# Kernel tuning notes

Hardware: AMD Instinct MI355X
Metric: run time of the kernel (lower is better)

The kernel has to match this reference:

```python
import jax, jax.numpy as jnp
import numpy as np

B, N, C, H = 4, 2048, 1024, 16
HD = C // H  # head_dim = 64


def setup_inputs() -> dict:
    key = jax.random.key(0)
    ks = jax.random.split(key, 16)
    s = 0.02
    return {
        "x": jax.random.normal(ks[0], (B, N, C), dtype=jnp.float32),
        # qkv_proj: Linear(C, 3C): weight (3C, C), bias (3C,)
        "W_qkv": jax.random.normal(ks[1], (3 * C, C), dtype=jnp.float32) * s,
        "b_qkv": jax.random.normal(ks[2], (3 * C,), dtype=jnp.float32) * s,
        # out_proj: Linear(C, C)
        "W_out": jax.random.normal(ks[3], (C, C), dtype=jnp.float32) * s,
        "b_out": jax.random.normal(ks[4], (C,), dtype=jnp.float32) * s,
        # dynamically-reassigned position bias: shape (1, N, H, H) per the code's
        # (B, num_heads=N, seq_len=H, seq_len=H) score tensor
        "pos_bias": jax.random.normal(ks[5], (1, N, H, H), dtype=jnp.float32) * 0.01,
        # conv_proj: Linear(C, C)
        "W_cp": jax.random.normal(ks[6], (C, C), dtype=jnp.float32) * s,
        "b_cp": jax.random.normal(ks[7], (C,), dtype=jnp.float32) * s,
        # pointwise Conv1d(C, C, k=1): weight (C, C) after squeezing kernel dim
        "W_pw": jax.random.normal(ks[8], (C, C), dtype=jnp.float32) * s,
        "b_pw": jax.random.normal(ks[9], (C,), dtype=jnp.float32) * s,
        # depthwise Conv1d(C, C, k=3, groups=C): weight (C, 3)
        "W_dw": jax.random.normal(ks[10], (C, 3), dtype=jnp.float32) * s,
        "b_dw": jax.random.normal(ks[11], (C,), dtype=jnp.float32) * s,
        # token_wise_proj: Linear(C, C)
        "W_tw": jax.random.normal(ks[12], (C, C), dtype=jnp.float32) * s,
        "b_tw": jax.random.normal(ks[13], (C,), dtype=jnp.float32) * s,
    }


def reference(x, W_qkv, b_qkv, W_out, b_out, pos_bias, W_cp, b_cp,
              W_pw, b_pw, W_dw, b_dw, W_tw, b_tw) -> jnp.ndarray:
    Bx, Nx, Cx = x.shape
    scale = HD ** -0.5
    # qkv -> (B, N, H, 3*HD), chunk into q,k,v of (B, N, H, HD).
    # NOTE: faithful to the torch code, heads stay on axis 2; the matmul
    # contracts head_dim giving (B, N, H, H) scores (attention over heads).
    qkv = (x @ W_qkv.T + b_qkv).reshape(Bx, Nx, H, 3 * HD)
    q, k, v = jnp.split(qkv, 3, axis=-1)
    scores = jnp.einsum('bnhd,bngd->bnhg', q, k) * scale + pos_bias
    attn = jax.nn.softmax(scores, axis=-1)
    attn_out = jnp.einsum('bnhg,bngd->bnhd', attn, v).reshape(Bx, Nx, Cx)
    attn_out = attn_out @ W_out.T + b_out

    # Convolutional branch
    xc = x @ W_cp.T + b_cp          # conv_proj
    xc = xc @ W_pw.T + b_pw          # pointwise conv (k=1) == linear over channels
    xp = jnp.pad(xc, ((0, 0), (1, 1), (0, 0)))  # pad seq for k=3, padding=1
    xc = (xp[:, :-2] * W_dw[:, 0] + xp[:, 1:-1] * W_dw[:, 1]
          + xp[:, 2:] * W_dw[:, 2] + b_dw)      # depthwise conv
    xc = xc @ W_tw.T + b_tw          # token_wise_proj

    return attn_out + xc
```

## Files before the change

kernel.cpp:

```cpp
#include <hip/hip_runtime.h>
#include <hip/hip_bf16.h>
#include <stdint.h>

typedef __bf16 bf16_t;
typedef __attribute__((ext_vector_type(8))) __bf16 bf16x8;
typedef __attribute__((ext_vector_type(4))) __bf16 bf16x4;
typedef __attribute__((ext_vector_type(4))) float floatx4;
typedef __attribute__((ext_vector_type(4))) _Float16 half4_t;

#define GLDS16(g, l)                                                          \
  __builtin_amdgcn_global_load_lds(                                           \
      (const __attribute__((address_space(1))) void*)(g),                     \
      (__attribute__((address_space(3))) void*)(l), 16, 0, 0)

template <int IT, int JT, typename OT>
__global__ __launch_bounds__(256) void gemm_bt(
    const bf16_t* __restrict__ A, const bf16_t* __restrict__ B,
    const float* __restrict__ bias, OT* __restrict__ C, int M, int N, int K) {
  constexpr int AROWS = 32 * IT;
  constexpr int BROWS = 32 * JT;
  constexpr int COLS = BROWS;
  constexpr int STAGE = (AROWS + BROWS) * 64;
  constexpr int EPI = (sizeof(OT) == 2) ? AROWS * COLS : 0;
  constexpr int SME = STAGE > EPI ? STAGE : EPI;
  __shared__ bf16_t sm[SME];
  bf16_t* As = sm;
  bf16_t* Bs = sm + AROWS * 64;

  const int tid = threadIdx.x;
  const int wave = tid >> 6;
  const int lane = tid & 63;
  const int quad = lane >> 4;
  const int l16 = lane & 15;
  const int m0 = blockIdx.x * AROWS;
  const int n0 = blockIdx.y * BROWS;
  const int wm = (wave >> 1) * (IT * 16);
  const int wn = (wave & 1) * (JT * 16);

  const int ra = wave * (8 * IT) + (lane >> 3);
  const int ga = ((lane & 7) ^ (ra & 7)) * 8;
  const int rb = wave * (8 * JT) + (lane >> 3);
  const int gb = ((lane & 7) ^ (rb & 7)) * 8;
  const bf16_t* Ab = A + (size_t)(m0 + ra) * K + ga;
  const bf16_t* Bb = B + (size_t)(n0 + rb) * K + gb;
  const int p0 = (quad ^ (l16 & 7)) * 8;

  floatx4 acc[IT][JT];
  const floatx4 zf = {0.f, 0.f, 0.f, 0.f};
#pragma unroll
  for (int i = 0; i < IT; ++i)
#pragma unroll
    for (int j = 0; j < JT; ++j) acc[i][j] = zf;

  for (int k0 = 0; k0 < K; k0 += 64) {
#pragma unroll
    for (int t = 0; t < IT; ++t)
      GLDS16(Ab + (size_t)(t * 8) * K + k0, As + (wave * (64 * IT) + t * 64) * 8);
#pragma unroll
    for (int t = 0; t < JT; ++t)
      GLDS16(Bb + (size_t)(t * 8) * K + k0, Bs + (wave * (64 * JT) + t * 64) * 8);
    __syncthreads();
#pragma unroll
    for (int ks = 0; ks < 2; ++ks) {
      const int ko = p0 ^ (ks * 32);
      bf16x8 af[IT], bfr[JT];
#pragma unroll
      for (int i = 0; i < IT; ++i)
        af[i] = *(const bf16x8*)(As + (wm + i * 16 + l16) * 64 + ko);
#pragma unroll
      for (int j = 0; j < JT; ++j)
        bfr[j] = *(const bf16x8*)(Bs + (wn + j * 16 + l16) * 64 + ko);
#pragma unroll
      for (int i = 0; i < IT; ++i)
#pragma unroll
        for (int j = 0; j < JT; ++j)
          acc[i][j] = __builtin_amdgcn_mfma_f32_16x16x32_bf16(
              bfr[j], af[i], acc[i][j], 0, 0, 0);
    }
    __syncthreads();
  }

  if constexpr (sizeof(OT) == 4) {
#pragma unroll
    for (int j = 0; j < JT; ++j) {
      const int colb = n0 + wn + j * 16 + quad * 4;
      floatx4 bv = zf;
      if (bias) bv = *(const floatx4*)(bias + colb);
#pragma unroll
      for (int i = 0; i < IT; ++i) {
        const int row = m0 + wm + i * 16 + l16;
        floatx4 v = acc[i][j] + bv;
        *(floatx4*)((float*)C + (size_t)row * N + colb) = v;
      }
    }
  } else {
    constexpr int SWZ = COLS / 32;
    constexpr int CPR = COLS / 8;
    constexpr int PASSES = (AROWS * CPR) / 256;
#pragma unroll
    for (int j = 0; j < JT; ++j) {
      const int colb = n0 + wn + j * 16 + quad * 4;
      floatx4 bv = zf;
      if (bias) bv = *(const floatx4*)(bias + colb);
      const int gcol = (wn + j * 16 + quad * 4) >> 2;
#pragma unroll
      for (int i = 0; i < IT; ++i) {
        const int rl = wm + i * 16 + l16;
        floatx4 v = acc[i][j] + bv;
        union {
          bf16_t b[4];
          uint2 u2;
        } pk;
        pk.b[0] = (bf16_t)v[0];
        pk.b[1] = (bf16_t)v[1];
        pk.b[2] = (bf16_t)v[2];
        pk.b[3] = (bf16_t)v[3];
        const int gsw = gcol ^ ((rl & 7) * SWZ);
        *(uint2*)(sm + rl * COLS + gsw * 4) = pk.u2;
      }
    }
    __syncthreads();
    bf16_t* Cb = (bf16_t*)C;
#pragma unroll
    for (int pass = 0; pass < PASSES; ++pass) {
      const int f = pass * 256 + tid;
      const int row = f / CPR;
      const int c16 = f % CPR;
      const int g0 = (2 * c16) ^ ((row & 7) * SWZ);
      uint4 v = *(const uint4*)(sm + row * COLS + g0 * 4);
      *(uint4*)(Cb + (size_t)(m0 + row) * N + n0 + c16 * 8) = v;
    }
  }
}

#define BAR8 asm volatile("s_barrier" ::: "memory")
#define VMCNT(n) asm volatile("s_waitcnt vmcnt(" #n ")" ::: "memory")

__global__ __launch_bounds__(512, 2) void gemm8p(
    const bf16_t* __restrict__ A, const bf16_t* __restrict__ B,
    const float* __restrict__ bias, bf16_t* __restrict__ C, int M, int N,
    int K) {
  __shared__ bf16_t sm8[65536];
  bf16_t* As = sm8;
  bf16_t* Bs = sm8 + 32768;

  const int tid = threadIdx.x;
  const int wave = tid >> 6, lane = tid & 63;
  const int l16 = lane & 15, quad = lane >> 4;
  const int wm = (wave >> 2) * 128, wn = (wave & 3) * 64;

  const int lin = blockIdx.y * gridDim.x + blockIdx.x;
  const int nwg = gridDim.x * gridDim.y;
  const int chunk = nwg >> 3;
  const int swz = (lin & 7) * chunk + (lin >> 3);
  const int bm = swz / gridDim.x;
  const int bn = swz % gridDim.x;
  const int m0 = bm << 8, n0 = bn << 8;

  const int srow = wave * 32 + (lane >> 2);
  const int kswz = ((lane & 3) * 8) ^ ((lane >> 5) << 4);
  const bf16_t* Ag = A + (size_t)(m0 + srow) * K + kswz;
  const bf16_t* Bg = B + (size_t)(n0 + srow) * K + kswz;
  const int sdst = wave * 1024;
  const size_t a16k = (size_t)K << 4;

  const int koe = (quad * 8) ^ ((l16 & 8) << 1);
  const int aoff = (wm + l16) * 32 + koe;
  const int boff = (wn + l16) * 32 + koe;

  floatx4 acc[8][4];
  const floatx4 zf = {0.f, 0.f, 0.f, 0.f};
#pragma unroll
  for (int i = 0; i < 8; ++i)
#pragma unroll
    for (int j = 0; j < 4; ++j) acc[i][j] = zf;

  bf16x8 af[4], bfr[4];

#define STG_A(buf, kh, TOFF)                                     \
  do {                                                           \
    bf16_t* _d = As + (buf)*16384 + (kh)*8192 + sdst;            \
    GLDS16(Ag + (TOFF) + (kh)*32, _d);                           \
    GLDS16(Ag + a16k + (TOFF) + (kh)*32, _d + 512);              \
  } while (0)
#define STG_B(buf, kh, TOFF)                                     \
  do {                                                           \
    bf16_t* _d = Bs + (buf)*16384 + (kh)*8192 + sdst;            \
    GLDS16(Bg + (TOFF) + (kh)*32, _d);                           \
    GLDS16(Bg + a16k + (TOFF) + (kh)*32, _d + 512);              \
  } while (0)
#define LDA4(buf, ks, mb)                                        \
  do {                                                           \
    const bf16_t* _p = As + (buf)*16384 + (ks)*8192 + aoff + (mb)*512; \
    af[0] = *(const bf16x8*)(_p);                                \
    af[1] = *(const bf16x8*)(_p + 512);                          \
    af[2] = *(const bf16x8*)(_p + 1024);                         \
    af[3] = *(const bf16x8*)(_p + 1536);                         \
  } while (0)
#define LDB4(buf, ks)                                            \
  do {                                                           \
    const bf16_t* _p = Bs + (buf)*16384 + (ks)*8192 + boff;      \
    bfr[0] = *(const bf16x8*)(_p);                               \
    bfr[1] = *(const bf16x8*)(_p + 512);                         \
    bfr[2] = *(const bf16x8*)(_p + 1024);                        \
    bfr[3] = *(const bf16x8*)(_p + 1536);                        \
  } while (0)
#define MFMA16(mb)                                               \
  do {                                                           \
    __builtin_amdgcn_s_setprio(1);                               \
    _Pragma("unroll") for (int _i = 0; _i < 4; ++_i)             \
        _Pragma("unroll") for (int _j = 0; _j < 4; ++_j)         \
            acc[(mb) + _i][_j] =                                 \
                __builtin_amdgcn_mfma_f32_16x16x32_bf16(         \
                    bfr[_j], af[_i], acc[(mb) + _i][_j], 0, 0, 0); \
    __builtin_amdgcn_s_setprio(0);                               \
  } while (0)

  STG_A(0, 0, 0);
  STG_A(0, 1, 0);
  STG_B(0, 0, 0);
  STG_B(0, 1, 0);
  STG_B(1, 0, 64);
  STG_A(1, 0, 64);
  STG_B(1, 1, 64);
  VMCNT(6);
  BAR8;

  const int NT = K >> 6;
  for (int it = 0; it < NT / 2 - 1; ++it) {
    LDA4(0, 0, 0); LDB4(0, 0); STG_A(1, 1, 64);            BAR8; MFMA16(0); BAR8;
    LDA4(0, 0, 4);             STG_B(0, 0, 128);           BAR8; MFMA16(4); BAR8;
    LDA4(0, 1, 0); LDB4(0, 1); STG_A(0, 0, 128);           BAR8; MFMA16(0); BAR8;
    LDA4(0, 1, 4);             STG_B(0, 1, 128); VMCNT(6); BAR8; MFMA16(4); BAR8;
    LDA4(1, 0, 0); LDB4(1, 0); STG_A(0, 1, 128);           BAR8; MFMA16(0); BAR8;
    LDA4(1, 0, 4);             STG_B(1, 0, 192);           BAR8; MFMA16(4); BAR8;
    LDA4(1, 1, 0); LDB4(1, 1); STG_A(1, 0, 192);           BAR8; MFMA16(0); BAR8;
    LDA4(1, 1, 4);             STG_B(1, 1, 192); VMCNT(6); BAR8; MFMA16(4); BAR8;
    Ag += 128;
    Bg += 128;
  }
  LDA4(0, 0, 0); LDB4(0, 0); STG_A(1, 1, 64); BAR8; MFMA16(0); BAR8;
  LDA4(0, 0, 4);                              BAR8; MFMA16(4); BAR8;
  LDA4(0, 1, 0); LDB4(0, 1);                  BAR8; MFMA16(0); BAR8;
  LDA4(0, 1, 4);             VMCNT(0);        BAR8; MFMA16(4); BAR8;
  LDA4(1, 0, 0); LDB4(1, 0);                  BAR8; MFMA16(0); BAR8;
  LDA4(1, 0, 4);                              BAR8; MFMA16(4); BAR8;
  LDA4(1, 1, 0); LDB4(1, 1);                  BAR8; MFMA16(0); BAR8;
  LDA4(1, 1, 4);                              BAR8; MFMA16(4); BAR8;

  const int crow_b = wm + l16;
#pragma unroll
  for (int nj = 0; nj < 4; ++nj) {
    const int colb = wn + nj * 16 + quad * 4;
    floatx4 bv = zf;
    if (bias) bv = *(const floatx4*)(bias + n0 + colb);
#pragma unroll
    for (int mi = 0; mi < 8; ++mi) {
      const int row = crow_b + mi * 16;
      floatx4 v = acc[mi][nj] + bv;
      union {
        bf16_t b[4];
        uint2 u2;
      } pk;
      pk.b[0] = (bf16_t)v[0];
      pk.b[1] = (bf16_t)v[1];
      pk.b[2] = (bf16_t)v[2];
      pk.b[3] = (bf16_t)v[3];
      const int cb = (colb * 2) ^ ((row & 31) << 4);
      *(uint2*)((char*)sm8 + row * 512 + cb) = pk.u2;
    }
  }
  __syncthreads();
#pragma unroll
  for (int pass = 0; pass < 16; ++pass) {
    const int flat = pass * 8192 + tid * 16;
    const int row = flat >> 9;
    const int cb = flat & 511;
    const int cbs = cb ^ ((row & 31) << 4);
    uint4 v = *(const uint4*)((char*)sm8 + row * 512 + cbs);
    *(uint4*)((char*)C + ((size_t)(m0 + row) * N + n0) * 2 + cb) = v;
  }
#undef STG_A
#undef STG_B
#undef LDA4
#undef LDB4
#undef MFMA16
}

__global__ __launch_bounds__(256) void prep2_k(
    const float* __restrict__ x, bf16_t* __restrict__ x_bf,
    const float* __restrict__ Wqkv, bf16_t* __restrict__ Wbig1,
    const float* __restrict__ Wpw, bf16_t* __restrict__ Wpw_bf,
    const float* __restrict__ Wout, const float* __restrict__ Wtw,
    bf16_t* __restrict__ Wbig2, const float* __restrict__ bqkv,
    float* __restrict__ bias1, const float* __restrict__ bout,
    const float* __restrict__ btw, float* __restrict__ bias2,
    const float* __restrict__ Wcp, bf16_t* __restrict__ WcpT,
    const float* __restrict__ bcp, const float* __restrict__ bpw) {
  __shared__ float t[32][33];
  const int b = blockIdx.x, tid = threadIdx.x;
  auto cvt4 = [](const float* in, bf16_t* out, int i) {
    floatx4 v = ((const floatx4*)in)[i];
    bf16x4 o;
    o[0] = (bf16_t)v[0];
    o[1] = (bf16_t)v[1];
    o[2] = (bf16_t)v[2];
    o[3] = (bf16_t)v[3];
    ((bf16x4*)out)[i] = o;
  };
  if (b < 8192) {
    cvt4(x, x_bf, b * 256 + tid);
  } else if (b < 11264) {
    cvt4(Wqkv, Wbig1, (b - 8192) * 256 + tid);
  } else if (b < 12288) {
    cvt4(Wpw, Wpw_bf, (b - 11264) * 256 + tid);
  } else if (b < 14336) {
    const bool second = b >= 13312;
    int i = (b - (second ? 13312 : 12288)) * 256 + tid;
    floatx4 v = ((const floatx4*)(second ? Wtw : Wout))[i];
    bf16x4 o;
    o[0] = (bf16_t)v[0];
    o[1] = (bf16_t)v[1];
    o[2] = (bf16_t)v[2];
    o[3] = (bf16_t)v[3];
    int row = i >> 8, c4 = i & 255;
    *(bf16x4*)(Wbig2 + (size_t)row * 2048 + (second ? 1024 : 0) + c4 * 4) = o;
  } else if (b < 14339) {
    int i = (b - 14336) * 256 + tid;
    if (i < 768) ((floatx4*)bias1)[i] = ((const floatx4*)bqkv)[i];
  } else if (b == 14339) {
    ((floatx4*)bias2)[tid] =
        ((const floatx4*)bout)[tid] + ((const floatx4*)btw)[tid];
  } else if (b < 15364) {
    const int tb = b - 14340;
    const int bx = (tb & 31) * 32, by = (tb >> 5) * 32;
    const int tx = tid & 31, ty = tid >> 5;
#pragma unroll
    for (int iq = 0; iq < 4; ++iq)
      t[ty + iq * 8][tx] = Wcp[(size_t)(by + ty + iq * 8) * 1024 + bx + tx];
    __syncthreads();
#pragma unroll
    for (int iq = 0; iq < 4; ++iq)
      WcpT[(size_t)(bx + ty + iq * 8) * 1024 + by + tx] =
          (bf16_t)t[tx][ty + iq * 8];
  } else {
    const int row = (b - 15364) * 4 + (tid >> 6);
    const int l = tid & 63;
    const float* wr = Wpw + (size_t)row * 1024;
    float s = 0.f;
    for (int j = l; j < 1024; j += 64) s += wr[j] * bcp[j];
#pragma unroll
    for (int o = 32; o > 0; o >>= 1) s += __shfl_down(s, o);
    if (l == 0) bias1[3072 + row] = s + bpw[row];
  }
}

static __device__ inline void exp8(uint32_t w0, uint32_t w1, uint32_t w2,
                                   uint32_t w3, float* f) {
  f[0] = __uint_as_float(w0 << 16);
  f[1] = __uint_as_float(w0 & 0xffff0000u);
  f[2] = __uint_as_float(w1 << 16);
  f[3] = __uint_as_float(w1 & 0xffff0000u);
  f[4] = __uint_as_float(w2 << 16);
  f[5] = __uint_as_float(w2 & 0xffff0000u);
  f[6] = __uint_as_float(w3 << 16);
  f[7] = __uint_as_float(w3 & 0xffff0000u);
}

__global__ __launch_bounds__(256) void mid_k(const bf16_t* __restrict__ G1,
                                             const float* __restrict__ pos,
                                             const float* __restrict__ Wdw,
                                             const float* __restrict__ bdw,
                                             bf16_t* __restrict__ Mid) {
  __shared__ bf16_t ost[4][16 * 68];
  const int tid = threadIdx.x;
  if (blockIdx.x < 2048) {
    const int wave = tid >> 6, lane = tid & 63;
    const int p = blockIdx.x * 4 + wave;
    const int l16 = lane & 15, quad = lane >> 4;
    const bf16_t* row = G1 + (size_t)p * 4096;
    const bf16_t* qb = row + l16 * 192 + quad * 8;

    bf16x8 q0 = *(const bf16x8*)(qb);
    bf16x8 q1 = *(const bf16x8*)(qb + 32);
    bf16x8 k0 = *(const bf16x8*)(qb + 64);
    bf16x8 k1 = *(const bf16x8*)(qb + 96);
    floatx4 S = {0.f, 0.f, 0.f, 0.f};
    S = __builtin_amdgcn_mfma_f32_16x16x32_bf16(k0, q0, S, 0, 0, 0);
    S = __builtin_amdgcn_mfma_f32_16x16x32_bf16(k1, q1, S, 0, 0, 0);

    const floatx4 pb = *(const floatx4*)(pos + (size_t)(p & 2047) * 256 +
                                         l16 * 16 + quad * 4);
    float v[4];
#pragma unroll
    for (int r = 0; r < 4; ++r) v[r] = S[r] * 0.125f + pb[r];

    float m = fmaxf(fmaxf(v[0], v[1]), fmaxf(v[2], v[3]));
    m = fmaxf(m, __shfl_xor(m, 16));
    m = fmaxf(m, __shfl_xor(m, 32));
    float e[4], sum = 0.f;
#pragma unroll
    for (int r = 0; r < 4; ++r) {
      e[r] = __expf(v[r] - m);
      sum += e[r];
    }
    sum += __shfl_xor(sum, 16);
    sum += __shfl_xor(sum, 32);
    const float inv = 1.0f / sum;
    half4_t pa;
#pragma unroll
    for (int r = 0; r < 4; ++r) pa[r] = (_Float16)(e[r] * inv);

    const bf16_t* vb_base = row + 128 + l16;
    const floatx4 zf = {0.f, 0.f, 0.f, 0.f};
    floatx4 o[4];
#pragma unroll
    for (int t = 0; t < 4; ++t) {
      half4_t vb;
#pragma unroll
      for (int j = 0; j < 4; ++j)
        vb[j] = (_Float16)(float)vb_base[(quad * 4 + j) * 192 + t * 16];
      o[t] = __builtin_amdgcn_mfma_f32_16x16x16f16(pa, vb, zf, 0, 0, 0);
    }

    bf16_t* ow = ost[wave];
#pragma unroll
    for (int r = 0; r < 4; ++r)
#pragma unroll
      for (int t = 0; t < 4; ++t)
        ow[(quad * 4 + r) * 68 + t * 16 + l16] = (bf16_t)o[t][r];
    const int h2 = lane >> 2, m4 = lane & 3;
    const bf16_t* srcp = ow + h2 * 68 + m4 * 16;
    uint2 a0 = *(const uint2*)(srcp);
    uint2 a1 = *(const uint2*)(srcp + 4);
    uint2 a2 = *(const uint2*)(srcp + 8);
    uint2 a3 = *(const uint2*)(srcp + 12);
    uint4 s0 = {a0.x, a0.y, a1.x, a1.y};
    uint4 s1 = {a2.x, a2.y, a3.x, a3.y};
    uint4* dst = (uint4*)(Mid + (size_t)p * 2048 + h2 * 64 + m4 * 16);
    dst[0] = s0;
    dst[1] = s1;
  } else {
    const bf16_t* in = G1 + 3072;
    bf16_t* out = Mid + 1024;
    const int item = (blockIdx.x - 2048) * 256 + tid;
    const int cc = item & 127, rowg = item >> 7;
    const int c0 = cc * 8;
    float w0[8], w1[8], w2[8], bb[8];
#pragma unroll
    for (int c = 0; c < 8; ++c) {
      w0[c] = Wdw[(c0 + c) * 3];
      w1[c] = Wdw[(c0 + c) * 3 + 1];
      w2[c] = Wdw[(c0 + c) * 3 + 2];
      bb[c] = bdw[c0 + c];
    }
#pragma unroll
    for (int jr = 0; jr < 4; ++jr) {
      const int tt = rowg * 4 + jr;
      const int n = tt & 2047;
      const bf16_t* ip = in + (size_t)tt * 4096 + c0;
      const uint4 z4 = {0, 0, 0, 0};
      uint4 um = (n > 0) ? *(const uint4*)(ip - 4096) : z4;
      uint4 uc = *(const uint4*)(ip);
      uint4 up = (n < 2047) ? *(const uint4*)(ip + 4096) : z4;
      float fm[8], fc[8], fp[8];
      exp8(um.x, um.y, um.z, um.w, fm);
      exp8(uc.x, uc.y, uc.z, uc.w, fc);
      exp8(up.x, up.y, up.z, up.w, fp);
      union {
        bf16_t b[8];
        uint4 u;
      } pk;
#pragma unroll
      for (int c = 0; c < 8; ++c)
        pk.b[c] =
            (bf16_t)(bb[c] + fm[c] * w0[c] + fc[c] * w1[c] + fp[c] * w2[c]);
      *(uint4*)(out + (size_t)tt * 2048 + c0) = pk.u;
    }
  }
}

extern "C" void kernel_launch(void* const* d_in, const int* in_sizes, int n_in,
                              void* d_out, int out_size, void* d_ws,
                              size_t ws_size, hipStream_t stream) {
  (void)in_sizes; (void)n_in; (void)out_size; (void)ws_size;
  const float* x = (const float*)d_in[0];
  const float* Wqkv = (const float*)d_in[1];
  const float* bqkv = (const float*)d_in[2];
  const float* Wout = (const float*)d_in[3];
  const float* bout = (const float*)d_in[4];
  const float* pos = (const float*)d_in[5];
  const float* Wcp = (const float*)d_in[6];
  const float* bcp = (const float*)d_in[7];
  const float* Wpw = (const float*)d_in[8];
  const float* bpw = (const float*)d_in[9];
  const float* Wdw = (const float*)d_in[10];
  const float* bdw = (const float*)d_in[11];
  const float* Wtw = (const float*)d_in[12];
  const float* btw = (const float*)d_in[13];
  float* out = (float*)d_out;

  char* ws = (char*)d_ws;
  const size_t MB = 1024ull * 1024ull;
  bf16_t* x_bf = (bf16_t*)(ws + 0);
  bf16_t* Wbig1 = (bf16_t*)(ws + 16 * MB);
  bf16_t* WcpT = (bf16_t*)(ws + 24 * MB);
  bf16_t* Wpw_bf = (bf16_t*)(ws + 26 * MB);
  bf16_t* Mid = (bf16_t*)(ws + 0);
  bf16_t* Wbig2 = (bf16_t*)(ws + 32 * MB);
  float* bias1 = (float*)(ws + 36 * MB);
  float* bias2 = (float*)(ws + 36 * MB + 65536);
  bf16_t* G1out = (bf16_t*)(ws + 37 * MB);

  prep2_k<<<15620, 256, 0, stream>>>(x, x_bf, Wqkv, Wbig1, Wpw, Wpw_bf, Wout,
                                     Wtw, Wbig2, bqkv, bias1, bout, btw, bias2,
                                     Wcp, WcpT, bcp, bpw);

  gemm_bt<2, 2, bf16_t><<<dim3(16, 16), 256, 0, stream>>>(
      Wpw_bf, WcpT, nullptr, Wbig1 + (size_t)3072 * 1024, 1024, 1024, 1024);

  gemm8p<<<dim3(16, 32), 512, 0, stream>>>(x_bf, Wbig1, bias1, G1out, 8192,
                                           4096, 1024);

  mid_k<<<3072, 256, 0, stream>>>(G1out, pos, Wdw, bdw, Mid);

  gemm_bt<4, 4, float><<<dim3(64, 8), 256, 0, stream>>>(Mid, Wbig2, bias2,
                                                        out, 8192, 1024, 2048);
}
```

Measured before the change: 276.8 us.

## Replace fine-grained interleaved GEMM pipeline with coarse double-buffered stages, drop tile swizzle

Rewrites the main loop of the 256x256 bf16 GEMM. The old schedule had many barriers per iteration, each interleaving partial LDS fragment loads with partial global-to-LDS staging. The new one computes a whole 64-wide K tile from one buffer, then refills that buffer with a full tile while the other buffer is consumed next. It also removes the XCD-aware workgroup swizzle in favour of a direct blockIdx mapping. This cuts barrier count and keeps more A fragments in registers, but overlaps global loads with MFMA less finely and may lose L2 locality across XCDs.

Result: no change. 277.2 us (+0.2%).

```diff
diff --git a/kernel.cpp b/kernel.cpp
--- a/kernel.cpp
+++ b/kernel.cpp
@@ -149,13 +149,7 @@
   const int l16 = lane & 15, quad = lane >> 4;
   const int wm = (wave >> 2) * 128, wn = (wave & 3) * 64;
 
-  const int lin = blockIdx.y * gridDim.x + blockIdx.x;
-  const int nwg = gridDim.x * gridDim.y;
-  const int chunk = nwg >> 3;
-  const int swz = (lin & 7) * chunk + (lin >> 3);
-  const int bm = swz / gridDim.x;
-  const int bn = swz % gridDim.x;
-  const int m0 = bm << 8, n0 = bn << 8;
+  const int m0 = blockIdx.y << 8, n0 = blockIdx.x << 8;
 
   const int srow = wave * 32 + (lane >> 2);
   const int kswz = ((lane & 3) * 8) ^ ((lane >> 5) << 4);
@@ -175,78 +169,103 @@
 #pragma unroll
     for (int j = 0; j < 4; ++j) acc[i][j] = zf;
 
-  bf16x8 af[4], bfr[4];
-
-#define STG_A(buf, kh, TOFF)                                     \
+#define STG_A(buf, kh)                                           \
   do {                                                           \
     bf16_t* _d = As + (buf)*16384 + (kh)*8192 + sdst;            \
-    GLDS16(Ag + (TOFF) + (kh)*32, _d);                           \
-    GLDS16(Ag + a16k + (TOFF) + (kh)*32, _d + 512);              \
+    GLDS16(Ag + (kh)*32, _d);                                    \
+    GLDS16(Ag + a16k + (kh)*32, _d + 512);                       \
   } while (0)
-#define STG_B(buf, kh, TOFF)                                     \
+#define STG_B(buf, kh)                                           \
   do {                                                           \
     bf16_t* _d = Bs + (buf)*16384 + (kh)*8192 + sdst;            \
-    GLDS16(Bg + (TOFF) + (kh)*32, _d);                           \
-    GLDS16(Bg + a16k + (TOFF) + (kh)*32, _d + 512);              \
+    GLDS16(Bg + (kh)*32, _d);                                    \
+    GLDS16(Bg + a16k + (kh)*32, _d + 512);                       \
   } while (0)
-#define LDA4(buf, ks, mb)                                        \
+#define STG4(buf)                                                \
   do {                                                           \
-    const bf16_t* _p = As + (buf)*16384 + (ks)*8192 + aoff + (mb)*512; \
-    af[0] = *(const bf16x8*)(_p);                                \
-    af[1] = *(const bf16x8*)(_p + 512);                          \
-    af[2] = *(const bf16x8*)(_p + 1024);                         \
-    af[3] = *(const bf16x8*)(_p + 1536);                         \
+    STG_A(buf, 0);                                               \
+    STG_A(buf, 1);                                               \
+    STG_B(buf, 0);                                               \
+    STG_B(buf, 1);                                               \
+    Ag += 64;                                                    \
+    Bg += 64;                                                    \
   } while (0)
-#define LDB4(buf, ks)                                            \
-  do {                                                           \
-    const bf16_t* _p = Bs + (buf)*16384 + (ks)*8192 + boff;      \
-    bfr[0] = *(const bf16x8*)(_p);                               \
-    bfr[1] = *(const bf16x8*)(_p + 512);                         \
-    bfr[2] = *(const bf16x8*)(_p + 1024);                        \
-    bfr[3] = *(const bf16x8*)(_p + 1536);                        \
+
+#define KHALF(buf, kh)                                                    \
+  do {                                                                    \
+    const bf16_t* _pb = Bs + (buf)*16384 + (kh)*8192 + boff;              \
+    const bf16_t* _pa = As + (buf)*16384 + (kh)*8192 + aoff;              \
+    bf16x8 bfr0 = *(const bf16x8*)(_pb);                                  \
+    bf16x8 bfr1 = *(const bf16x8*)(_pb + 512);                            \
+    bf16x8 bfr2 = *(const bf16x8*)(_pb + 1024);                           \
+    bf16x8 bfr3 = *(const bf16x8*)(_pb + 1536);                           \
+    bf16x8 afa[4], afb[4];                                                \
+    _Pragma("unroll") for (int _i = 0; _i < 4; ++_i)                      \
+        afa[_i] = *(const bf16x8*)(_pa + _i * 512);                       \
+    _Pragma("unroll") for (int _i = 0; _i < 4; ++_i)                      \
+        afb[_i] = *(const bf16x8*)(_pa + 2048 + _i * 512);                \
+    __builtin_amdgcn_s_setprio(1);                                        \
+    _Pragma("unroll") for (int _i = 0; _i < 4; ++_i) {                    \
+      acc[_i][0] = __builtin_amdgcn_mfma_f32_16x16x32_bf16(               \
+          bfr0, afa[_i], acc[_i][0], 0, 0, 0);                            \
+      acc[_i][1] = __builtin_amdgcn_mfma_f32_16x16x32_bf16(               \
+          bfr1, afa[_i], acc[_i][1], 0, 0, 0);                            \
+      acc[_i][2] = __builtin_amdgcn_mfma_f32_16x16x32_bf16(               \
+          bfr2, afa[_i], acc[_i][2], 0, 0, 0);                            \
+      acc[_i][3] = __builtin_amdgcn_mfma_f32_16x16x32_bf16(               \
+          bfr3, afa[_i], acc[_i][3], 0, 0, 0);                            \
+    }                                                                     \
+    _Pragma("unroll") for (int _i = 0; _i < 4; ++_i) {                    \
+      acc[4 + _i][0] = __builtin_amdgcn_mfma_f32_16x16x32_bf16(           \
+          bfr0, afb[_i], acc[4 + _i][0], 0, 0, 0);                        \
+      acc[4 + _i][1] = __builtin_amdgcn_mfma_f32_16x16x32_bf16(           \
+          bfr1, afb[_i], acc[4 + _i][1], 0, 0, 0);                        \
+      acc[4 + _i][2] = __builtin_amdgcn_mfma_f32_16x16x32_bf16(           \
+          bfr2, afb[_i], acc[4 + _i][2], 0, 0, 0);                        \
+      acc[4 + _i][3] = __builtin_amdgcn_mfma_f32_16x16x32_bf16(           \
+          bfr3, afb[_i], acc[4 + _i][3], 0, 0, 0);                        \
+    }                                                                     \
+    __builtin_amdgcn_s_setprio(0);                                        \
   } while (0)
-#define MFMA16(mb)                                               \
-  do {                                                           \
-    __builtin_amdgcn_s_setprio(1);                               \
-    _Pragma("unroll") for (int _i = 0; _i < 4; ++_i)             \
-        _Pragma("unroll") for (int _j = 0; _j < 4; ++_j)         \
-            acc[(mb) + _i][_j] =                                 \
-                __builtin_amdgcn_mfma_f32_16x16x32_bf16(         \
-                    bfr[_j], af[_i], acc[(mb) + _i][_j], 0, 0, 0); \
-    __builtin_amdgcn_s_setprio(0);                               \
-  } while (0)
-
-  STG_A(0, 0, 0);
-  STG_A(0, 1, 0);
-  STG_B(0, 0, 0);
-  STG_B(0, 1, 0);
-  STG_B(1, 0, 64);
-  STG_A(1, 0, 64);
-  STG_B(1, 1, 64);
-  VMCNT(6);
+
+  STG_A(0, 0);
+  STG_A(0, 1);
+  STG_B(0, 0);
+  STG_B(0, 1);
+  Ag += 64;
+  Bg += 64;
+  STG_A(1, 0);
+  STG_A(1, 1);
+  STG_B(1, 0);
+  STG_B(1, 1);
+  Ag += 64;
+  Bg += 64;
+  VMCNT(8);
   BAR8;
 
   const int NT = K >> 6;
   for (int it = 0; it < NT / 2 - 1; ++it) {
-    LDA4(0, 0, 0); LDB4(0, 0); STG_A(1, 1, 64);            BAR8; MFMA16(0); BAR8;
-    LDA4(0, 0, 4);             STG_B(0, 0, 128);           BAR8; MFMA16(4); BAR8;
-    LDA4(0, 1, 0); LDB4(0, 1); STG_A(0, 0, 128);           BAR8; MFMA16(0); BAR8;
-    LDA4(0, 1, 4);             STG_B(0, 1, 128); VMCNT(6); BAR8; MFMA16(4); BAR8;
-    LDA4(1, 0, 0); LDB4(1, 0); STG_A(0, 1, 128);           BAR8; MFMA16(0); BAR8;
-    LDA4(1, 0, 4);             STG_B(1, 0, 192);           BAR8; MFMA16(4); BAR8;
-    LDA4(1, 1, 0); LDB4(1, 1); STG_A(1, 0, 192);           BAR8; MFMA16(0); BAR8;
-    LDA4(1, 1, 4);             STG_B(1, 1, 192); VMCNT(6); BAR8; MFMA16(4); BAR8;
-    Ag += 128;
-    Bg += 128;
-  }
-  LDA4(0, 0, 0); LDB4(0, 0); STG_A(1, 1, 64); BAR8; MFMA16(0); BAR8;
-  LDA4(0, 0, 4);                              BAR8; MFMA16(4); BAR8;
-  LDA4(0, 1, 0); LDB4(0, 1);                  BAR8; MFMA16(0); BAR8;
-  LDA4(0, 1, 4);             VMCNT(0);        BAR8; MFMA16(4); BAR8;
-  LDA4(1, 0, 0); LDB4(1, 0);                  BAR8; MFMA16(0); BAR8;
-  LDA4(1, 0, 4);                              BAR8; MFMA16(4); BAR8;
-  LDA4(1, 1, 0); LDB4(1, 1);                  BAR8; MFMA16(0); BAR8;
-  LDA4(1, 1, 4);                              BAR8; MFMA16(4); BAR8;
+    KHALF(0, 0);
+    KHALF(0, 1);
+    BAR8;
+    STG4(0);
+    VMCNT(8);
+    BAR8;
+    KHALF(1, 0);
+    KHALF(1, 1);
+    BAR8;
+    STG4(1);
+    VMCNT(8);
+    BAR8;
+  }
+  KHALF(0, 0);
+  KHALF(0, 1);
+  BAR8;
+  VMCNT(0);
+  BAR8;
+  KHALF(1, 0);
+  KHALF(1, 1);
+  __syncthreads();
 
   const int crow_b = wm + l16;
 #pragma unroll
@@ -282,9 +301,8 @@
   }
 #undef STG_A
 #undef STG_B
-#undef LDA4
-#undef LDB4
-#undef MFMA16
+#undef STG4
+#undef KHALF
 }
 
 __global__ __launch_bounds__(256) void prep2_k(
```

## Replace final output GEMM with pipelined 512-thread direct-to-LDS kernel

Applied to the files above, without the earlier changes.

Adds gemm8p2, a 512-thread, 128x256-tile bf16 GEMM with fp32 output. It stages A/B through LDS using global_load_lds double buffering, swizzled layout, explicit vmcnt/barrier scheduling and raised wave priority around the MFMA blocks, and it replaces gemm_bt<4,4,float> for the final Mid x Wbig2 projection. The goal is to overlap global loads with MFMA work and raise compute density. In exchange, the grid drops to 256 workgroups and bias and fp32 results are written straight from registers without LDS staging.

Result: faster. 265.9 us (-3.9%).

```diff
diff --git a/kernel.cpp b/kernel.cpp
--- a/kernel.cpp
+++ b/kernel.cpp
@@ -12,6 +12,9 @@
   __builtin_amdgcn_global_load_lds(                                           \
       (const __attribute__((address_space(1))) void*)(g),                     \
       (__attribute__((address_space(3))) void*)(l), 16, 0, 0)
+
+#define BAR8 asm volatile("s_barrier" ::: "memory")
+#define VMCNT(n) asm volatile("s_waitcnt vmcnt(" #n ")" ::: "memory")
 
 template <int IT, int JT, typename OT>
 __global__ __launch_bounds__(256) void gemm_bt(
@@ -133,9 +136,6 @@
   }
 }
 
-#define BAR8 asm volatile("s_barrier" ::: "memory")
-#define VMCNT(n) asm volatile("s_waitcnt vmcnt(" #n ")" ::: "memory")
-
 __global__ __launch_bounds__(512, 2) void gemm8p(
     const bf16_t* __restrict__ A, const bf16_t* __restrict__ B,
     const float* __restrict__ bias, bf16_t* __restrict__ C, int M, int N,
@@ -285,6 +285,108 @@
 #undef LDA4
 #undef LDB4
 #undef MFMA16
+}
+
+__global__ __launch_bounds__(512, 2) void gemm8p2(
+    const bf16_t* __restrict__ A, const bf16_t* __restrict__ B,
+    const float* __restrict__ bias, float* __restrict__ C, int M, int N,
+    int K) {
+  __shared__ bf16_t sm2[49152];
+  bf16_t* As = sm2;
+  bf16_t* Bs = sm2 + 16384;
+
+  const int tid = threadIdx.x;
+  const int wave = tid >> 6, lane = tid & 63;
+  const int l16 = lane & 15, quad = lane >> 4;
+  const int wm = (wave >> 2) * 64, wn = (wave & 3) * 64;
+  const int m0 = blockIdx.y << 7, n0 = blockIdx.x << 8;
+
+  const int srA = wave * 16 + (lane >> 2);
+  const int srB = wave * 32 + (lane >> 2);
+  const int kswz = ((lane & 3) * 8) ^ ((lane >> 5) << 4);
+  const bf16_t* Ag = A + (size_t)(m0 + srA) * K + kswz;
+  const bf16_t* Bg = B + (size_t)(n0 + srB) * K + kswz;
+  const size_t b16k = (size_t)K << 4;
+
+  const int koe = (quad * 8) ^ ((l16 & 8) << 1);
+  const int aoff = (wm + l16) * 32 + koe;
+  const int boff = (wn + l16) * 32 + koe;
+
+  floatx4 acc[4][4];
+  const floatx4 zf = {0.f, 0.f, 0.f, 0.f};
+#pragma unroll
+  for (int i = 0; i < 4; ++i)
+#pragma unroll
+    for (int j = 0; j < 4; ++j) acc[i][j] = zf;
+
+  bf16x8 af[4], bfr[4];
+
+#define SA2(buf, kh, TOFF)                                                 \
+  GLDS16(Ag + (TOFF) + (kh)*32, As + (buf)*8192 + (kh)*4096 + wave * 512)
+#define SB2(buf, kh, TOFF)                                                 \
+  do {                                                                     \
+    bf16_t* _d = Bs + (buf)*16384 + (kh)*8192 + wave * 1024;               \
+    GLDS16(Bg + (TOFF) + (kh)*32, _d);                                     \
+    GLDS16(Bg + b16k + (TOFF) + (kh)*32, _d + 512);                        \
+  } while (0)
+#define LD2(buf, kh)                                                       \
+  do {                                                                     \
+    const bf16_t* _pa = As + (buf)*8192 + (kh)*4096 + aoff;                \
+    const bf16_t* _pb = Bs + (buf)*16384 + (kh)*8192 + boff;               \
+    _Pragma("unroll") for (int _i = 0; _i < 4; ++_i)                       \
+        af[_i] = *(const bf16x8*)(_pa + _i * 512);                         \
+    _Pragma("unroll") for (int _j = 0; _j < 4; ++_j)                       \
+        bfr[_j] = *(const bf16x8*)(_pb + _j * 512);                        \
+  } while (0)
+#define MM2                                                                \
+  do {                                                                     \
+    __builtin_amdgcn_s_setprio(1);                                         \
+    _Pragma("unroll") for (int _i = 0; _i < 4; ++_i)                       \
+        _Pragma("unroll") for (int _j = 0; _j < 4; ++_j)                   \
+            acc[_i][_j] = __builtin_amdgcn_mfma_f32_16x16x32_bf16(         \
+                bfr[_j], af[_i], acc[_i][_j], 0, 0, 0);                    \
+    __builtin_amdgcn_s_setprio(0);                                         \
+  } while (0)
+
+  SA2(0, 0, 0);
+  SB2(0, 0, 0);
+  SA2(0, 1, 0);
+  SB2(0, 1, 0);
+  SA2(1, 0, 64);
+  SB2(1, 0, 64);
+  VMCNT(3);
+  BAR8;
+
+  const int NT = K >> 6;
+  for (int it = 0; it < NT / 2 - 1; ++it) {
+    LD2(0, 0); SA2(1, 1, 64);  SB2(1, 1, 64);            BAR8; MM2; BAR8;
+    LD2(0, 1); SA2(0, 0, 128); SB2(0, 0, 128); VMCNT(3); BAR8; MM2; BAR8;
+    LD2(1, 0); SA2(0, 1, 128); SB2(0, 1, 128);           BAR8; MM2; BAR8;
+    LD2(1, 1); SA2(1, 0, 192); SB2(1, 0, 192); VMCNT(3); BAR8; MM2; BAR8;
+    Ag += 128;
+    Bg += 128;
+  }
+  LD2(0, 0); SA2(1, 1, 64); SB2(1, 1, 64); BAR8; MM2; BAR8;
+  LD2(0, 1); VMCNT(0);                     BAR8; MM2; BAR8;
+  LD2(1, 0);                               BAR8; MM2; BAR8;
+  LD2(1, 1);                                     MM2;
+
+#pragma unroll
+  for (int j = 0; j < 4; ++j) {
+    const int colb = n0 + wn + j * 16 + quad * 4;
+    floatx4 bv = zf;
+    if (bias) bv = *(const floatx4*)(bias + colb);
+#pragma unroll
+    for (int i = 0; i < 4; ++i) {
+      const int row = m0 + wm + i * 16 + l16;
+      floatx4 v = acc[i][j] + bv;
+      *(floatx4*)(C + (size_t)row * N + colb) = v;
+    }
+  }
+#undef SA2
+#undef SB2
+#undef LD2
+#undef MM2
 }
 
 __global__ __launch_bounds__(256) void prep2_k(
@@ -524,6 +626,6 @@
 
   mid_k<<<3072, 256, 0, stream>>>(G1out, pos, Wdw, bdw, Mid);
 
-  gemm_bt<4, 4, float><<<dim3(64, 8), 256, 0, stream>>>(Mid, Wbig2, bias2,
-                                                        out, 8192, 1024, 2048);
+  gemm8p2<<<dim3(4, 64), 512, 0, stream>>>(Mid, Wbig2, bias2, out, 8192, 1024,
+                                           2048);
 }
```
